# Kernel tuning notes

Hardware: AMD Instinct MI355X
Metric: run time of the kernel (lower is better)

Reference implementation:

```python
import math
import jax, jax.numpy as jnp
import numpy as np

B, L, N, DM, H = 4, 12, 512, 64, 8
D = DM // H
FACTOR = 5  # args.spatial_factor


def setup_inputs() -> dict:
    key = jax.random.key(0)
    ks = jax.random.split(key, 6)
    s = 1.0 / math.sqrt(DM)
    return {
        "queries": jax.random.normal(ks[0], (B, L, N, DM), jnp.float32),
        "keys": jax.random.normal(ks[1], (B, L, N, DM), jnp.float32),
        "values": jax.random.normal(ks[2], (B, L, N, DM), jnp.float32),
        "Wq": jax.random.normal(ks[3], (DM, DM), jnp.float32) * s,
        "bq": jnp.zeros((DM,), jnp.float32),
        "Wk": jax.random.normal(ks[4], (DM, DM), jnp.float32) * s,
        "bk": jnp.zeros((DM,), jnp.float32),
        "Wv": jax.random.normal(ks[5], (DM, DM), jnp.float32) * s,
        "bv": jnp.zeros((DM,), jnp.float32),
    }


def reference(queries, keys, values, Wq, bq, Wk, bk, Wv, bv):
    # QKV projections (torch nn.Linear), then split heads and move to [B,H,N,L,D]
    q = jnp.transpose((queries @ Wq + bq).reshape(B, L, N, H, D), (0, 3, 2, 1, 4))
    k = jnp.transpose((keys @ Wk + bk).reshape(B, L, N, H, D), (0, 3, 2, 1, 4))
    v = jnp.transpose((values @ Wv + bv).reshape(B, L, N, H, D), (0, 3, 2, 1, 4))

    sample_k = min(FACTOR * int(np.ceil(np.log(N))), N)  # = n_top = effect_N

    # --- _prob_QK: random K sampling over the N (spatial) axis ---
    idx = jax.random.randint(jax.random.key(42), (N, sample_k), 0, N)  # [N, sk]
    K_sample = k[:, :, idx]                       # [B,H,N,sk,L,D] gather
    # Q.unsqueeze(-2) @ K_sample^T -> [B,H,N,L,sk], then transposed to [B,H,L,N,sk]
    qk_s = jnp.einsum('bhnld,bhnsld->bhlns', q, K_sample)
    M = qk_s.max(axis=-1) - qk_s.sum(axis=-1) / N  # sparsity measure [B,H,L,N]
    _, M_top = jax.lax.top_k(M, sample_k)          # [B,H,L,n_top]

    q_t = jnp.transpose(q, (0, 1, 3, 2, 4))        # [B,H,L,N,D]
    Q_red = jnp.take_along_axis(q_t, M_top[..., None], axis=3)  # [B,H,L,n_top,D]
    scores = jnp.einsum('bhltd,bhnld->bhltn', Q_red, k) / math.sqrt(D)

    # --- context: mean of V over nodes, overwritten at top queries ---
    attn = jax.nn.softmax(scores, axis=-1)                        # [B,H,L,n_top,N]
    attn_ret = jnp.einsum('bhltn,bhnld->bhltd', attn, v)          # [B,H,L,n_top,D]
    ctx = jnp.broadcast_to(v.mean(axis=2)[:, :, :, None, :], (B, H, L, N, D))
    bi = jnp.arange(B)[:, None, None, None]
    hi = jnp.arange(H)[None, :, None, None]
    li = jnp.arange(L)[None, None, :, None]
    ctx = ctx.at[bi, hi, li, M_top].set(attn_ret)                 # scatter-write

    out = jnp.transpose(ctx, (0, 2, 3, 1, 4)).reshape(B, L, N, DM)
    return out  # dropout p=0.0 -> identity
```

## Files before the change

### kernel.cpp

```cpp
#include <hip/hip_runtime.h>
#include <stdint.h>
#include <math.h>

#define BB 4
#define LL 12
#define NN 512
#define DMM 64
#define HH 8
#define DD 8
#define SK 35
#define IDX_TOTAL (NN*SK)
#define PADK 12

__device__ __forceinline__ void tf2x32(uint32_t k0, uint32_t k1, uint32_t x0, uint32_t x1,
                                       uint32_t& o0, uint32_t& o1) {
  const uint32_t ks2 = k0 ^ k1 ^ 0x1BD11BDAu;
  uint32_t a = x0 + k0, b = x1 + k1;
#define TF_R(r) { a += b; b = (b << (r)) | (b >> (32 - (r))); b ^= a; }
  TF_R(13) TF_R(15) TF_R(26) TF_R(6)
  a += k1;  b += ks2 + 1u;
  TF_R(17) TF_R(29) TF_R(16) TF_R(24)
  a += ks2; b += k0 + 2u;
  TF_R(13) TF_R(15) TF_R(26) TF_R(6)
  a += k0;  b += k1 + 3u;
  TF_R(17) TF_R(29) TF_R(16) TF_R(24)
  a += k1;  b += ks2 + 4u;
  TF_R(13) TF_R(15) TF_R(26) TF_R(6)
  a += ks2; b += k0 + 5u;
#undef TF_R
  o0 = a; o1 = b;
}

__global__ __launch_bounds__(256) void proj_idx_kernel(
    const float* __restrict__ Xq, const float* __restrict__ Xk, const float* __restrict__ Xv,
    const float* __restrict__ Wq_, const float* __restrict__ Wk_, const float* __restrict__ Wv_,
    const float* __restrict__ bq_, const float* __restrict__ bk_, const float* __restrict__ bv_,
    float* __restrict__ Oq, float* __restrict__ Ok, float* __restrict__ Ov,
    int* __restrict__ idxT) {
  const int tz = blockIdx.y;
  if (tz == 3) {
    int gid = blockIdx.x * 256 + threadIdx.x;
    if (gid < IDX_TOTAL) {
      int r = gid & (NN - 1);
      int s = gid >> 9;
      uint32_t ka, kb;
      tf2x32(0u, 42u, 0u, 1u, ka, kb);
      uint32_t b1, b2;
      tf2x32(ka, kb, 0u, (uint32_t)(r * SK + s), b1, b2);
      idxT[gid] = (int)((b1 ^ b2) & (uint32_t)(NN - 1));
    }
    return;
  }
  const float* X    = (tz == 0) ? Xq  : (tz == 1) ? Xk  : Xv;
  const float* W    = (tz == 0) ? Wq_ : (tz == 1) ? Wk_ : Wv_;
  const float* bias = (tz == 0) ? bq_ : (tz == 1) ? bk_ : bv_;
  float* O          = (tz == 0) ? Oq  : (tz == 1) ? Ok  : Ov;

  __shared__ __align__(16) float Ws[64][64];
  __shared__ __align__(16) float Xs[64][68];
  __shared__ float bs[64];

  const int tid = threadIdx.x;
  const size_t rowBase = (size_t)blockIdx.x * 64;
  const float* Xb = X + rowBase * 64;
  #pragma unroll
  for (int i = 0; i < 4; ++i) {
    int idx = tid + i*256;
    ((float4*)Ws)[idx] = ((const float4*)W)[idx];
    int r = idx >> 4, c = (idx & 15) << 2;
    *(float4*)&Xs[r][c] = ((const float4*)Xb)[idx];
  }
  if (tid < 64) bs[tid] = bias[tid];
  __syncthreads();

  const int hcol = tid & 7;
  const int rb   = tid >> 3;
  float4 bv0 = *(float4*)&bs[hcol*8];
  float4 bv1 = *(float4*)&bs[hcol*8+4];
  float acc[2][8];
  #pragma unroll
  for (int i = 0; i < 2; ++i) {
    acc[i][0]=bv0.x; acc[i][1]=bv0.y; acc[i][2]=bv0.z; acc[i][3]=bv0.w;
    acc[i][4]=bv1.x; acc[i][5]=bv1.y; acc[i][6]=bv1.z; acc[i][7]=bv1.w;
  }
  #pragma unroll 8
  for (int m = 0; m < 64; ++m) {
    float4 w0 = *(const float4*)&Ws[m][hcol*8];
    float4 w1 = *(const float4*)&Ws[m][hcol*8+4];
    float x0 = Xs[rb][m];
    float x1 = Xs[rb+32][m];
    acc[0][0]=fmaf(x0,w0.x,acc[0][0]); acc[0][1]=fmaf(x0,w0.y,acc[0][1]);
    acc[0][2]=fmaf(x0,w0.z,acc[0][2]); acc[0][3]=fmaf(x0,w0.w,acc[0][3]);
    acc[0][4]=fmaf(x0,w1.x,acc[0][4]); acc[0][5]=fmaf(x0,w1.y,acc[0][5]);
    acc[0][6]=fmaf(x0,w1.z,acc[0][6]); acc[0][7]=fmaf(x0,w1.w,acc[0][7]);
    acc[1][0]=fmaf(x1,w0.x,acc[1][0]); acc[1][1]=fmaf(x1,w0.y,acc[1][1]);
    acc[1][2]=fmaf(x1,w0.z,acc[1][2]); acc[1][3]=fmaf(x1,w0.w,acc[1][3]);
    acc[1][4]=fmaf(x1,w1.x,acc[1][4]); acc[1][5]=fmaf(x1,w1.y,acc[1][5]);
    acc[1][6]=fmaf(x1,w1.z,acc[1][6]); acc[1][7]=fmaf(x1,w1.w,acc[1][7]);
  }
  #pragma unroll
  for (int i = 0; i < 2; ++i) {
    size_t R = rowBase + rb + 32*i;
    int bI = (int)(R / (LL*NN));
    int lI = (int)((R / NN) % LL);
    int nI = (int)(R % NN);
    size_t off = ((((size_t)bI*HH + hcol)*LL + lI)*NN + nI)*DD;
    *(float4*)&O[off]     = make_float4(acc[i][0],acc[i][1],acc[i][2],acc[i][3]);
    *(float4*)&O[off + 4] = make_float4(acc[i][4],acc[i][5],acc[i][6],acc[i][7]);
  }
}

__global__ __launch_bounds__(512) void fused_kernel(
    const float* __restrict__ Qt, const float* __restrict__ Kt,
    const float* __restrict__ Vt, const int* __restrict__ idxT,
    float* __restrict__ out) {
  const int bid = blockIdx.x;
  const int l = bid % LL;
  const int h = (bid / LL) % HH;
  const int b = bid / (LL*HH);
  const int tid = threadIdx.x;
  const int wave = tid >> 6, lane = tid & 63;

  __shared__ __align__(16) float Ks[NN][PADK];
  __shared__ __align__(16) float Vs[NN][PADK];
  __shared__ __align__(16) uint64_t keys[NN];
  __shared__ int sel[NN];
  __shared__ int topIdxL[SK + 1];
  __shared__ __align__(16) float attnOut[SK][8];
  __shared__ __align__(16) float redD[8][64][8];
  __shared__ __align__(16) float vm[8];

  int (*partial)[4] = (int(*)[4])redD;

  const size_t slabOff = (size_t)bid * (NN*DD);

  {
    const float4* kg = (const float4*)(Kt + slabOff);
    float4 a = kg[tid*2], c = kg[tid*2+1];
    *(float4*)&Ks[tid][0] = a; *(float4*)&Ks[tid][4] = c;
  }
  const float4* qp = (const float4*)(Qt + slabOff + (size_t)tid*DD);
  float4 qa = qp[0], qb = qp[1];
  int jv[SK];
  const int* gi = idxT + tid;
  #pragma unroll
  for (int s = 0; s < SK; ++s) jv[s] = gi[s*NN];
  sel[tid] = -1;
  __syncthreads();

  {
    float mx = -INFINITY, sm = 0.f;
    #pragma unroll
    for (int s = 0; s < SK; ++s) {
      int j = jv[s];
      float4 c0 = *(const float4*)&Ks[j][0];
      float4 c1 = *(const float4*)&Ks[j][4];
      float dot = qa.x*c0.x + qa.y*c0.y + qa.z*c0.z + qa.w*c0.w
                + qb.x*c1.x + qb.y*c1.y + qb.z*c1.z + qb.w*c1.w;
      mx = fmaxf(mx, dot);
      sm += dot;
    }
    float m = mx - sm * (1.0f/NN);
    uint32_t u = __float_as_uint(m);
    uint32_t fk = (u & 0x80000000u) ? ~u : (u | 0x80000000u);
    keys[tid] = ((uint64_t)fk << 32) | (uint32_t)(NN - 1 - tid);
  }
  __syncthreads();

  {
    const int qgrp = tid >> 7, li = tid & 127;
    uint64_t k0 = keys[li], k1 = keys[li+128], k2 = keys[li+256], k3 = keys[li+384];
    const ulonglong2* kq = (const ulonglong2*)(keys + qgrp*128);
    int c0 = 0, c1 = 0, c2 = 0, c3 = 0;
    #pragma unroll 8
    for (int jb = 0; jb < 64; ++jb) {
      ulonglong2 kv = kq[jb];
      c0 += (kv.x > k0) ? 1 : 0; c0 += (kv.y > k0) ? 1 : 0;
      c1 += (kv.x > k1) ? 1 : 0; c1 += (kv.y > k1) ? 1 : 0;
      c2 += (kv.x > k2) ? 1 : 0; c2 += (kv.y > k2) ? 1 : 0;
      c3 += (kv.x > k3) ? 1 : 0; c3 += (kv.y > k3) ? 1 : 0;
    }
    partial[li][qgrp]     = c0;
    partial[li+128][qgrp] = c1;
    partial[li+256][qgrp] = c2;
    partial[li+384][qgrp] = c3;
  }
  const float4* vg = (const float4*)(Vt + slabOff) + tid*2;
  float4 v0 = vg[0], v1 = vg[1];
  __syncthreads();

  {
    int4 pc = *(const int4*)&partial[tid][0];
    int cnt = pc.x + pc.y + pc.z + pc.w;
    if (cnt < SK) { topIdxL[cnt] = tid; sel[tid] = cnt; }
  }
  __syncthreads();
  *(float4*)&Vs[tid][0] = v0;
  *(float4*)&Vs[tid][4] = v1;
  __syncthreads();

  if (wave == 0) {
    float a[8] = {0,0,0,0,0,0,0,0};
    #pragma unroll
    for (int j = 0; j < 8; ++j) {
      int n = lane + 64*j;
      float4 w0 = *(const float4*)&Vs[n][0];
      float4 w1 = *(const float4*)&Vs[n][4];
      a[0]+=w0.x; a[1]+=w0.y; a[2]+=w0.z; a[3]+=w0.w;
      a[4]+=w1.x; a[5]+=w1.y; a[6]+=w1.z; a[7]+=w1.w;
    }
    *(float4*)&redD[0][lane][0] = make_float4(a[0],a[1],a[2],a[3]);
    *(float4*)&redD[0][lane][4] = make_float4(a[4],a[5],a[6],a[7]);
    const int d = lane & 7, g = lane >> 3;
    float s = 0.f;
    #pragma unroll
    for (int k = 0; k < 8; ++k) s += redD[0][g*8+k][d];
    s += __shfl_xor(s, 8); s += __shfl_xor(s, 16); s += __shfl_xor(s, 32);
    if (lane < 8) vm[lane] = s * (1.0f/NN);
  } else {
    const int base = (wave - 1) * 5;
    auto do_rows = [&](int t1, int t2, bool has2) {
      const int n1 = topIdxL[t1];
      const int n2 = has2 ? topIdxL[t2] : n1;
      const float4* q1p = (const float4*)(Qt + slabOff + (size_t)n1*DD);
      const float4* q2p = (const float4*)(Qt + slabOff + (size_t)n2*DD);
      float4 q1a = q1p[0], q1b = q1p[1];
      float4 q2a = q2p[0], q2b = q2p[1];
      float p1[8], p2[8];
      float mx1 = -INFINITY, mx2 = -INFINITY;
      #pragma unroll
      for (int j = 0; j < 8; ++j) {
        int n = lane + 64*j;
        float4 ca = *(const float4*)&Ks[n][0];
        float4 cb = *(const float4*)&Ks[n][4];
        float s1 = q1a.x*ca.x + q1a.y*ca.y + q1a.z*ca.z + q1a.w*ca.w
                 + q1b.x*cb.x + q1b.y*cb.y + q1b.z*cb.z + q1b.w*cb.w;
        float s2 = q2a.x*ca.x + q2a.y*ca.y + q2a.z*ca.z + q2a.w*ca.w
                 + q2b.x*cb.x + q2b.y*cb.y + q2b.z*cb.z + q2b.w*cb.w;
        s1 *= 0.35355339059327373f;
        s2 *= 0.35355339059327373f;
        p1[j] = s1; p2[j] = s2;
        mx1 = fmaxf(mx1, s1); mx2 = fmaxf(mx2, s2);
      }
      #pragma unroll
      for (int off = 32; off >= 1; off >>= 1) {
        mx1 = fmaxf(mx1, __shfl_xor(mx1, off));
        mx2 = fmaxf(mx2, __shfl_xor(mx2, off));
      }
      float sum1 = 0.f, sum2 = 0.f;
      #pragma unroll
      for (int j = 0; j < 8; ++j) {
        p1[j] = __expf(p1[j] - mx1); sum1 += p1[j];
        p2[j] = __expf(p2[j] - mx2); sum2 += p2[j];
      }
      #pragma unroll
      for (int off = 32; off >= 1; off >>= 1) {
        sum1 += __shfl_xor(sum1, off);
        sum2 += __shfl_xor(sum2, off);
      }
      float a1[8] = {0,0,0,0,0,0,0,0}, a2[8] = {0,0,0,0,0,0,0,0};
      #pragma unroll
      for (int j = 0; j < 8; ++j) {
        int n = lane + 64*j;
        float4 va = *(const float4*)&Vs[n][0];
        float4 vb = *(const float4*)&Vs[n][4];
        float w1 = p1[j], w2 = p2[j];
        a1[0]=fmaf(w1,va.x,a1[0]); a1[1]=fmaf(w1,va.y,a1[1]);
        a1[2]=fmaf(w1,va.z,a1[2]); a1[3]=fmaf(w1,va.w,a1[3]);
        a1[4]=fmaf(w1,vb.x,a1[4]); a1[5]=fmaf(w1,vb.y,a1[5]);
        a1[6]=fmaf(w1,vb.z,a1[6]); a1[7]=fmaf(w1,vb.w,a1[7]);
        a2[0]=fmaf(w2,va.x,a2[0]); a2[1]=fmaf(w2,va.y,a2[1]);
        a2[2]=fmaf(w2,va.z,a2[2]); a2[3]=fmaf(w2,va.w,a2[3]);
        a2[4]=fmaf(w2,vb.x,a2[4]); a2[5]=fmaf(w2,vb.y,a2[5]);
        a2[6]=fmaf(w2,vb.z,a2[6]); a2[7]=fmaf(w2,vb.w,a2[7]);
      }
      const int d = lane & 7, g = lane >> 3;
      {
        *(float4*)&redD[wave][lane][0] = make_float4(a1[0],a1[1],a1[2],a1[3]);
        *(float4*)&redD[wave][lane][4] = make_float4(a1[4],a1[5],a1[6],a1[7]);
        float s = 0.f;
        #pragma unroll
        for (int k = 0; k < 8; ++k) s += redD[wave][g*8+k][d];
        s += __shfl_xor(s, 8); s += __shfl_xor(s, 16); s += __shfl_xor(s, 32);
        if (lane < 8) attnOut[t1][lane] = s * (1.0f / sum1);
      }
      if (has2) {
        *(float4*)&redD[wave][lane][0] = make_float4(a2[0],a2[1],a2[2],a2[3]);
        *(float4*)&redD[wave][lane][4] = make_float4(a2[4],a2[5],a2[6],a2[7]);
        float s = 0.f;
        #pragma unroll
        for (int k = 0; k < 8; ++k) s += redD[wave][g*8+k][d];
        s += __shfl_xor(s, 8); s += __shfl_xor(s, 16); s += __shfl_xor(s, 32);
        if (lane < 8) attnOut[t2][lane] = s * (1.0f / sum2);
      }
    };
    do_rows(base, base + 1, true);
    do_rows(base + 2, base + 3, true);
    do_rows(base + 4, base + 4, false);
  }
  __syncthreads();

  {
    int t = sel[tid];
    float4 o0, o1;
    if (t >= 0) { o0 = *(const float4*)&attnOut[t][0]; o1 = *(const float4*)&attnOut[t][4]; }
    else        { o0 = *(const float4*)&vm[0];         o1 = *(const float4*)&vm[4]; }
    float* ob = out + ((size_t)(b*LL + l)*NN + tid)*DMM + h*DD;
    *(float4*)&ob[0] = o0;
    *(float4*)&ob[4] = o1;
  }
}

extern "C" void kernel_launch(void* const* d_in, const int* in_sizes, int n_in,
                              void* d_out, int out_size, void* d_ws, size_t ws_size,
                              hipStream_t stream) {
  const float* q  = (const float*)d_in[0];
  const float* k  = (const float*)d_in[1];
  const float* v  = (const float*)d_in[2];
  const float* Wq = (const float*)d_in[3];
  const float* bq = (const float*)d_in[4];
  const float* Wk = (const float*)d_in[5];
  const float* bk = (const float*)d_in[6];
  const float* Wv = (const float*)d_in[7];
  const float* bv = (const float*)d_in[8];
  float* out = (float*)d_out;

  const size_t slab = (size_t)BB*HH*LL*NN*DD;
  float* qT = (float*)d_ws;
  float* kT = qT + slab;
  float* vT = kT + slab;
  int*   idxT = (int*)(vT + slab);

  proj_idx_kernel<<<dim3((BB*LL*NN)/64, 4), 256, 0, stream>>>(
      q, k, v, Wq, Wk, Wv, bq, bk, bv, qT, kT, vT, idxT);
  fused_kernel<<<BB*HH*LL, 512, 0, stream>>>(qT, kT, vT, idxT, out);
}
```

Measured before the change: 56.27 us.

## Drop V shared-memory staging, chunk index loads, and raise occupancy bound

Removes the Vs shared-memory tile and reads V directly from global memory (via L1/L2) in the mean and attention-weighted sum loops. This drops a barrier and cuts LDS use per block. The 35 sampled indices are now loaded in 5 chunks of 7 instead of all at once, which lowers register pressure. Launch bounds now request 6 blocks per CU. The cost is repeated global reads of V by each wave, and less overlap between the index load latency and compute.

```diff
diff --git a/kernel.cpp b/kernel.cpp
--- a/kernel.cpp
+++ b/kernel.cpp
@@ -110,7 +110,7 @@
   }
 }
 
-__global__ __launch_bounds__(512) void fused_kernel(
+__global__ __launch_bounds__(512, 6) void fused_kernel(
     const float* __restrict__ Qt, const float* __restrict__ Kt,
     const float* __restrict__ Vt, const int* __restrict__ idxT,
     float* __restrict__ out) {
@@ -122,7 +122,6 @@
   const int wave = tid >> 6, lane = tid & 63;
 
   __shared__ __align__(16) float Ks[NN][PADK];
-  __shared__ __align__(16) float Vs[NN][PADK];
   __shared__ __align__(16) uint64_t keys[NN];
   __shared__ int sel[NN];
   __shared__ int topIdxL[SK + 1];
@@ -141,24 +140,27 @@
   }
   const float4* qp = (const float4*)(Qt + slabOff + (size_t)tid*DD);
   float4 qa = qp[0], qb = qp[1];
-  int jv[SK];
-  const int* gi = idxT + tid;
-  #pragma unroll
-  for (int s = 0; s < SK; ++s) jv[s] = gi[s*NN];
   sel[tid] = -1;
   __syncthreads();
 
   {
+    const int* gi = idxT + tid;
     float mx = -INFINITY, sm = 0.f;
-    #pragma unroll
-    for (int s = 0; s < SK; ++s) {
-      int j = jv[s];
-      float4 c0 = *(const float4*)&Ks[j][0];
-      float4 c1 = *(const float4*)&Ks[j][4];
-      float dot = qa.x*c0.x + qa.y*c0.y + qa.z*c0.z + qa.w*c0.w
-                + qb.x*c1.x + qb.y*c1.y + qb.z*c1.z + qb.w*c1.w;
-      mx = fmaxf(mx, dot);
-      sm += dot;
+    #pragma unroll 1
+    for (int c = 0; c < 5; ++c) {
+      int jc[7];
+      #pragma unroll
+      for (int t = 0; t < 7; ++t) jc[t] = gi[(c*7 + t)*NN];
+      #pragma unroll
+      for (int t = 0; t < 7; ++t) {
+        int j = jc[t];
+        float4 c0 = *(const float4*)&Ks[j][0];
+        float4 c1 = *(const float4*)&Ks[j][4];
+        float dot = qa.x*c0.x + qa.y*c0.y + qa.z*c0.z + qa.w*c0.w
+                  + qb.x*c1.x + qb.y*c1.y + qb.z*c1.z + qb.w*c1.w;
+        mx = fmaxf(mx, dot);
+        sm += dot;
+      }
     }
     float m = mx - sm * (1.0f/NN);
     uint32_t u = __float_as_uint(m);
@@ -185,8 +187,6 @@
     partial[li+256][qgrp] = c2;
     partial[li+384][qgrp] = c3;
   }
-  const float4* vg = (const float4*)(Vt + slabOff) + tid*2;
-  float4 v0 = vg[0], v1 = vg[1];
   __syncthreads();
 
   {
@@ -195,19 +195,17 @@
     if (cnt < SK) { topIdxL[cnt] = tid; sel[tid] = cnt; }
   }
   __syncthreads();
-  *(float4*)&Vs[tid][0] = v0;
-  *(float4*)&Vs[tid][4] = v1;
-  __syncthreads();
+
+  const float4* vp = (const float4*)(Vt + slabOff);
 
   if (wave == 0) {
     float a[8] = {0,0,0,0,0,0,0,0};
     #pragma unroll
     for (int j = 0; j < 8; ++j) {
-      int n = lane + 64*j;
-      float4 w0 = *(const float4*)&Vs[n][0];
-      float4 w1 = *(const float4*)&Vs[n][4];
-      a[0]+=w0.x; a[1]+=w0.y; a[2]+=w0.z; a[3]+=w0.w;
-      a[4]+=w1.x; a[5]+=w1.y; a[6]+=w1.z; a[7]+=w1.w;
+      const float4* vr = vp + (size_t)(lane + 64*j)*2;
+      float4 v0 = vr[0], v1 = vr[1];
+      a[0]+=v0.x; a[1]+=v0.y; a[2]+=v0.z; a[3]+=v0.w;
+      a[4]+=v1.x; a[5]+=v1.y; a[6]+=v1.z; a[7]+=v1.w;
     }
     *(float4*)&redD[0][lane][0] = make_float4(a[0],a[1],a[2],a[3]);
     *(float4*)&redD[0][lane][4] = make_float4(a[4],a[5],a[6],a[7]);
@@ -262,8 +260,7 @@
       #pragma unroll
       for (int j = 0; j < 8; ++j) {
         int n = lane + 64*j;
-        float4 va = *(const float4*)&Vs[n][0];
-        float4 vb = *(const float4*)&Vs[n][4];
+        float4 va = vp[n*2], vb = vp[n*2+1];
         float w1 = p1[j], w2 = p2[j];
         a1[0]=fmaf(w1,va.x,a1[0]); a1[1]=fmaf(w1,va.y,a1[1]);
         a1[2]=fmaf(w1,va.z,a1[2]); a1[3]=fmaf(w1,va.w,a1[3]);
```

After: 122.7 us. 118% more time.
